# Kernel optimization log

Hardware: AMD Instinct MI355X
Metric: run time of the kernel (lower is better)

The kernel has to match this reference:

```python
import jax, jax.numpy as jnp
import numpy as np


def gcn_conv(x, edge_index, edge_weight, W, b):
    """PyG GCNConv: add self-loops (weight 1), symmetric normalization,
    linear transform, edge-weighted scatter-add aggregation, bias."""
    N = x.shape[0]
    src = jnp.concatenate([edge_index[0], jnp.arange(N, dtype=edge_index.dtype)])
    dst = jnp.concatenate([edge_index[1], jnp.arange(N, dtype=edge_index.dtype)])
    ew = jnp.concatenate([edge_weight, jnp.ones((N,), dtype=edge_weight.dtype)])
    # deg over destination nodes (source_to_target flow)
    deg = jax.ops.segment_sum(ew, dst, num_segments=N)
    dinv = jnp.where(deg > 0, deg ** -0.5, 0.0).astype(x.dtype)
    norm = dinv[src] * ew * dinv[dst]          # [E+N]
    xw = x @ W                                  # [N, out] linear first (cheaper)
    msgs = norm[:, None] * xw[src]              # [E+N, out]
    out = jax.ops.segment_sum(msgs, dst, num_segments=N)
    return out + b


def setup_inputs() -> dict:
    key = jax.random.key(0)
    ks = jax.random.split(key, 7)
    N, E, F_in, H, F_out = 100000, 1600000, 394, 256, 64
    x = jax.random.normal(ks[0], (N, F_in), dtype=jnp.float32)
    edge_index = jax.random.randint(ks[1], (2, E), 0, N, dtype=jnp.int32)
    edge_weight = jax.random.uniform(ks[2], (E,), dtype=jnp.float32)
    W1 = jax.random.normal(ks[3], (F_in, H), dtype=jnp.float32) * (1.0 / np.sqrt(F_in))
    b1 = jnp.zeros((H,), dtype=jnp.float32)
    W2 = jax.random.normal(ks[4], (H, F_out), dtype=jnp.float32) * (1.0 / np.sqrt(H))
    b2 = jnp.zeros((F_out,), dtype=jnp.float32)
    return {"x": x, "edge_index": edge_index, "edge_weight": edge_weight,
            "W1": W1, "b1": b1, "W2": W2, "b2": b2}


def reference(x, edge_index, edge_weight, W1, b1, W2, b2):
    h = gcn_conv(x, edge_index, edge_weight, W1, b1)
    h = jax.nn.relu(h)
    # F.dropout(training=self.training) is identity in eval mode
    out = gcn_conv(h, edge_index, edge_weight, W2, b2)
    return out
```

## Files before the change

kernel.cpp:

```cpp
#include <hip/hip_runtime.h>
#include <hip/hip_bf16.h>
#include <hip/hip_fp16.h>
#include <type_traits>


typedef _Float16 f16x8 __attribute__((ext_vector_type(8)));
typedef float f32x4 __attribute__((ext_vector_type(4)));

#define DEG_MASK ((1ull << 42) - 1)

__device__ inline void async_copy16(const void* g, void* l) {
    __builtin_amdgcn_global_load_lds(
        (const __attribute__((address_space(1))) void*)g,
        (__attribute__((address_space(3))) void*)l, 16, 0, 0);
}


__global__ __launch_bounds__(256) void setup(unsigned long long* packed, int N,
                                             const float* __restrict__ W1,
                                             __half* __restrict__ WT1,
                                             int K1, int N1, int Kpad1,
                                             const float* __restrict__ W2,
                                             __half* __restrict__ WT2,
                                             int K2, int N2, int Kpad2,
                                             int G0, int G1) {
    int b = blockIdx.x;
    if (b < G0) {
        int i = b * 256 + threadIdx.x;
        if (i < N) packed[i] = 0ull;
    } else if (b < G1) {
        int idx = (b - G0) * 256 + threadIdx.x;
        int total = N1 * Kpad1;
        if (idx < total) {
            int n = idx / Kpad1, k = idx % Kpad1;
            float v = (k < K1) ? W1[(size_t)k * N1 + n] : 0.0f;
            WT1[idx] = __float2half(v);
        }
    } else {
        int idx = (b - G1) * 256 + threadIdx.x;
        int total = N2 * Kpad2;
        if (idx < total) {
            int n = idx / Kpad2, k = idx % Kpad2;
            float v = (k < K2) ? W2[(size_t)k * N2 + n] : 0.0f;
            WT2[idx] = __float2half(v);
        }
    }
}

__global__ __launch_bounds__(256) void accum_deg_hist(const int* __restrict__ dst,
                                                      const float* __restrict__ ew,
                                                      unsigned long long* packed, int E) {
    int e = blockIdx.x * 256 + threadIdx.x;
    if (e < E) {
        int d = dst[e];
        unsigned long long add =
            (1ull << 42) + (unsigned long long)(ew[e] * 4294967296.0f);
        atomicAdd(&packed[d], add);
    }
}

#define SCAN_TILE 2048

__global__ __launch_bounds__(256) void scan1(const unsigned long long* __restrict__ packed,
                                             int* __restrict__ rowptr,
                                             float* __restrict__ dinv,
                                             int* __restrict__ bsums, int N) {
    __shared__ int tmp[256];
    int t = threadIdx.x;
    int base = blockIdx.x * SCAN_TILE + t * 8;
    int v[8], s = 0;
#pragma unroll
    for (int j = 0; j < 8; ++j) {
        int idx = base + j;
        if (idx < N) {
            unsigned long long pv = packed[idx];
            v[j] = (int)(pv >> 42);
            dinv[idx] = rsqrtf(1.0f + (float)(pv & DEG_MASK) * (1.0f / 4294967296.0f));
        } else v[j] = 0;
        s += v[j];
    }
    tmp[t] = s;
    __syncthreads();
#pragma unroll
    for (int off = 1; off < 256; off <<= 1) {
        int u = (t >= off) ? tmp[t - off] : 0;
        __syncthreads();
        tmp[t] += u;
        __syncthreads();
    }
    int run = tmp[t] - s;
#pragma unroll
    for (int j = 0; j < 8; ++j) {
        if (base + j < N) rowptr[base + j] = run;
        run += v[j];
    }
    if (t == 255) bsums[blockIdx.x] = tmp[255];
}

__global__ __launch_bounds__(256) void scan2(int* bsums, int* rowptr, int NB, int N, int E) {
    __shared__ int tmp[256];
    int t = threadIdx.x;
    int v = (t < NB) ? bsums[t] : 0;
    tmp[t] = v;
    __syncthreads();
#pragma unroll
    for (int off = 1; off < 256; off <<= 1) {
        int u = (t >= off) ? tmp[t - off] : 0;
        __syncthreads();
        tmp[t] += u;
        __syncthreads();
    }
    if (t < NB) bsums[t] = tmp[t] - v;
    if (t == 0) rowptr[N] = E;
}

__global__ __launch_bounds__(256) void scan3(int* rowptr, int* cursor,
                                             const int* __restrict__ bsums, int N) {
    int base = blockIdx.x * SCAN_TILE + threadIdx.x * 8;
    int off = bsums[blockIdx.x];
#pragma unroll
    for (int j = 0; j < 8; ++j)
        if (base + j < N) {
            int v = rowptr[base + j] + off;
            rowptr[base + j] = v;
            cursor[base + j] = v;
        }
}

template <int BM, int BN, int WARPS_M, int WARPS_N, int NT>
__global__ __launch_bounds__(NT) void gemm1_fill(const float* __restrict__ Ax,
                                                 const __half* __restrict__ BT,
                                                 __half* __restrict__ C,
                                                 int M, int K, int Kpad,
                                                 int GF,
                                                 const int* __restrict__ src,
                                                 const int* __restrict__ dst,
                                                 const float* __restrict__ ew,
                                                 const float* __restrict__ dinv,
                                                 int* __restrict__ cursor,
                                                 int2* __restrict__ cv, int E) {
    const int WM = BM / WARPS_M, WN = BN / WARPS_N;
    const int FM = WM / 16, FN = WN / 16;
    const int ACH = BM * 4;
    const int BCH = BN * 4;
    static_assert(ACH == NT, "1 A-chunk per thread");
    static_assert(BCH == 2 * NT, "2 B-chunks per thread");
    __shared__ __align__(16) __half lds[2][(ACH + BCH) * 8];

    if ((int)blockIdx.x < GF) {
        int e = blockIdx.x * NT + threadIdx.x;
        if (e < E) {
            int d = dst[e], s = src[e];
            int pos = atomicAdd(&cursor[d], 1);
            float v = dinv[s] * ew[e];
            cv[pos] = make_int2(s, __float_as_int(v));
        }
        return;
    }

    int tid = threadIdx.x;
    int lane = tid & 63;
    int w = tid >> 6;
    int wr = w / WARPS_N, wc = w % WARPS_N;
    int bm = (blockIdx.x - GF) * BM;
    int lrow = lane & 15;
    int lslot = lane >> 4;

    int arow = tid >> 2, ap = tid & 3;
    int aslot = ap ^ ((arow >> 1) & 3);
    int agrow = bm + arow; if (agrow >= M) agrow = M - 1;
    const float* abase = Ax + (size_t)agrow * K;

    const __half* bsrc[2];
#pragma unroll
    for (int i = 0; i < 2; ++i) {
        int c = tid + i * NT;
        int row = c >> 2, p = c & 3;
        bsrc[i] = BT + (size_t)row * Kpad + (size_t)((p ^ ((row >> 1) & 3)) * 8);
    }

    f32x4 acc[FM][FN];
#pragma unroll
    for (int m = 0; m < FM; ++m)
#pragma unroll
        for (int n = 0; n < FN; ++n) acc[m][n] = (f32x4){0.f, 0.f, 0.f, 0.f};

    float2 ar[4];
    auto loadA = [&](int s) {
        int gk = s * 32 + aslot * 8;
        if (gk + 8 <= K) {
            const float* p = abase + gk;
            ar[0] = *(const float2*)p;
            ar[1] = *(const float2*)(p + 2);
            ar[2] = *(const float2*)(p + 4);
            ar[3] = *(const float2*)(p + 6);
        } else {
            float t[8];
#pragma unroll
            for (int j = 0; j < 8; ++j) t[j] = (gk + j < K) ? abase[gk + j] : 0.0f;
            ar[0] = make_float2(t[0], t[1]);
            ar[1] = make_float2(t[2], t[3]);
            ar[2] = make_float2(t[4], t[5]);
            ar[3] = make_float2(t[6], t[7]);
        }
    };
    auto writeA = [&](int buf) {
        union { __half2 h[4]; uint4 u; } pk;
#pragma unroll
        for (int j = 0; j < 4; ++j) pk.h[j] = __floats2half2_rn(ar[j].x, ar[j].y);
        *(uint4*)&lds[buf][(size_t)tid * 8] = pk.u;
    };
    auto stageB = [&](int buf) {
#pragma unroll
        for (int i = 0; i < 2; ++i) {
            async_copy16(bsrc[i], &lds[buf][(size_t)((tid & ~63) + (i + 1) * NT) * 8]);
            bsrc[i] += 32;
        }
    };

    auto compute = [&](int buf) {
        f16x8 af[FM], bf[FN];
#pragma unroll
        for (int m = 0; m < FM; ++m) {
            int row = wr * WM + m * 16 + lrow;
            int p = lslot ^ ((row >> 1) & 3);
            af[m] = *(const f16x8*)&lds[buf][(size_t)(row * 4 + p) * 8];
        }
#pragma unroll
        for (int n = 0; n < FN; ++n) {
            int row = wc * WN + n * 16 + lrow;
            int p = lslot ^ ((row >> 1) & 3);
            bf[n] = *(const f16x8*)&lds[buf][(size_t)(ACH + row * 4 + p) * 8];
        }
#pragma unroll
        for (int m = 0; m < FM; ++m)
#pragma unroll
            for (int n = 0; n < FN; ++n)
                acc[m][n] = __builtin_amdgcn_mfma_f32_16x16x32_f16(af[m], bf[n], acc[m][n], 0, 0, 0);
    };

    const int nsteps = Kpad / 32;
    loadA(0);
    stageB(0);
    asm volatile("s_waitcnt vmcnt(2)" ::: "memory");
    writeA(0);
    asm volatile("s_waitcnt vmcnt(0) lgkmcnt(0)" ::: "memory");
    __builtin_amdgcn_s_barrier();
    for (int s = 0; s < nsteps; ++s) {
        bool more = (s + 1 < nsteps);
        if (more) { loadA(s + 1); stageB((s + 1) & 1); }
        compute(s & 1);
        if (more) {
            asm volatile("s_waitcnt vmcnt(2)" ::: "memory");
            writeA((s + 1) & 1);
            asm volatile("s_waitcnt vmcnt(0) lgkmcnt(0)" ::: "memory");
        }
        __builtin_amdgcn_s_barrier();
    }

    __syncthreads();
    {
        const int LW = WN + 8;
        __half* tile = (__half*)lds + (size_t)w * 16 * LW;
        const int CPR = WN / 8;
        const int CHT = (16 * CPR) / 64;
#pragma unroll
        for (int m = 0; m < FM; ++m) {
            int rb = bm + wr * WM + m * 16;
#pragma unroll
            for (int n = 0; n < FN; ++n)
#pragma unroll
                for (int i = 0; i < 4; ++i)
                    tile[((lane >> 4) * 4 + i) * LW + n * 16 + (lane & 15)] =
                        __float2half(acc[m][n][i]);
#pragma unroll
            for (int c = 0; c < CHT; ++c) {
                int ch = lane + c * 64;
                int r = ch / CPR, cc = ch % CPR;
                uint4 v = *(uint4*)&tile[r * LW + cc * 8];
                int grow = rb + r;
                if (grow < M)
                    *(uint4*)&C[(size_t)grow * BN + wc * WN + cc * 8] = v;
            }
        }
    }
}

template <int BM, int BN, int WARPS_M, int WARPS_N, int NT>
__global__ __launch_bounds__(NT) void gemm_f16(const __half* __restrict__ Ah,
                                               const __half* __restrict__ BT,
                                               __half* __restrict__ C,
                                               int M, int Kpad) {
    const int WM = BM / WARPS_M, WN = BN / WARPS_N;
    const int FM = WM / 16, FN = WN / 16;
    const int ACH = BM * 4;
    const int BCH = BN * 4;
    const int TOTCH = ACH + BCH;
    const int CH = TOTCH / NT;
    static_assert(CH == 3, "vmcnt(3) hardcoded below");
    __shared__ __align__(16) __half lds[2][TOTCH * 8];

    int tid = threadIdx.x;
    int lane = tid & 63;
    int w = tid >> 6;
    int wr = w / WARPS_N, wc = w % WARPS_N;
    int bm = blockIdx.x * BM;
    int lrow = lane & 15;
    int lslot = lane >> 4;

    const __half* srcp[CH];
#pragma unroll
    for (int i = 0; i < CH; ++i) {
        int ch = tid + i * NT;
        if (ch < ACH) {
            int c = ch, row = c >> 2;
            int grow = bm + row;
            if (grow >= M) grow = M - 1;
            srcp[i] = Ah + (size_t)grow * Kpad + (size_t)(((c & 3) ^ ((row >> 1) & 3)) * 8);
        } else {
            int c = ch - ACH, row = c >> 2;
            srcp[i] = BT + (size_t)row * Kpad + (size_t)(((c & 3) ^ ((row >> 1) & 3)) * 8);
        }
    }

    f32x4 acc[FM][FN];
#pragma unroll
    for (int m = 0; m < FM; ++m)
#pragma unroll
        for (int n = 0; n < FN; ++n) acc[m][n] = (f32x4){0.f, 0.f, 0.f, 0.f};

    auto stage = [&](int buf) {
#pragma unroll
        for (int i = 0; i < CH; ++i) {
            async_copy16(srcp[i], &lds[buf][(size_t)((tid & ~63) + i * NT) * 8]);
            srcp[i] += 32;
        }
    };

    auto compute = [&](int buf) {
        f16x8 af[FM], bf[FN];
#pragma unroll
        for (int m = 0; m < FM; ++m) {
            int row = wr * WM + m * 16 + lrow;
            int p = lslot ^ ((row >> 1) & 3);
            af[m] = *(const f16x8*)&lds[buf][(size_t)(row * 4 + p) * 8];
        }
#pragma unroll
        for (int n = 0; n < FN; ++n) {
            int row = wc * WN + n * 16 + lrow;
            int p = lslot ^ ((row >> 1) & 3);
            bf[n] = *(const f16x8*)&lds[buf][(size_t)(ACH + row * 4 + p) * 8];
        }
#pragma unroll
        for (int m = 0; m < FM; ++m)
#pragma unroll
            for (int n = 0; n < FN; ++n)
                acc[m][n] = __builtin_amdgcn_mfma_f32_16x16x32_f16(af[m], bf[n], acc[m][n], 0, 0, 0);
    };

    const int nsteps = Kpad / 32;
    stage(0);
    for (int s = 0; s < nsteps; ++s) {
        if (s + 1 < nsteps) {
            stage((s + 1) & 1);
            asm volatile("s_waitcnt vmcnt(3)" ::: "memory");
        } else {
            asm volatile("s_waitcnt vmcnt(0)" ::: "memory");
        }
        __builtin_amdgcn_s_barrier();
        compute(s & 1);
        __builtin_amdgcn_s_barrier();
    }

    __syncthreads();
    {
        const int LW = WN + 8;
        __half* tile = (__half*)lds + (size_t)w * 16 * LW;
        const int CPR = WN / 8;
        const int CHT = (16 * CPR) / 64;
#pragma unroll
        for (int m = 0; m < FM; ++m) {
            int rb = bm + wr * WM + m * 16;
#pragma unroll
            for (int n = 0; n < FN; ++n)
#pragma unroll
                for (int i = 0; i < 4; ++i)
                    tile[((lane >> 4) * 4 + i) * LW + n * 16 + (lane & 15)] =
                        __float2half(acc[m][n][i]);
#pragma unroll
            for (int c = 0; c < CHT; ++c) {
                int ch = lane + c * 64;
                int r = ch / CPR, cc = ch % CPR;
                uint4 v = *(uint4*)&tile[r * LW + cc * 8];
                int grow = rb + r;
                if (grow < M)
                    *(uint4*)&C[(size_t)grow * BN + wc * WN + cc * 8] = v;
            }
        }
    }
}

template <int F, int LPN, int RELU, typename OutT>
__global__ __launch_bounds__(256) void gatherh(const int* __restrict__ rowptr,
                                               const int2* __restrict__ cv,
                                               const __half* __restrict__ xw,
                                               const float* __restrict__ dinv,
                                               const float* __restrict__ bias,
                                               OutT* __restrict__ out, int N) {
    const int NPB = 256 / LPN;
    int d = blockIdx.x * NPB + threadIdx.x / LPN;
    if (d >= N) return;
    int lane = threadIdx.x % LPN;

    float di = dinv[d];
    uint2 raw = *(const uint2*)(xw + (size_t)d * F + lane * 4);
    float2 u0 = __half22float2(*(__half2*)&raw.x);
    float2 u1 = __half22float2(*(__half2*)&raw.y);
    float a0 = di * u0.x, a1 = di * u0.y, a2 = di * u1.x, a3 = di * u1.y;
    float b0 = 0.f, b1 = 0.f, b2 = 0.f, b3 = 0.f;

    int p = rowptr[d], p1 = rowptr[d + 1];
    for (; p + 4 <= p1; p += 4) {
        int2 e0 = cv[p], e1 = cv[p + 1], e2 = cv[p + 2], e3 = cv[p + 3];
        uint2 r0 = *(const uint2*)(xw + (size_t)e0.x * F + lane * 4);
        uint2 r1 = *(const uint2*)(xw + (size_t)e1.x * F + lane * 4);
        uint2 r2 = *(const uint2*)(xw + (size_t)e2.x * F + lane * 4);
        uint2 r3 = *(const uint2*)(xw + (size_t)e3.x * F + lane * 4);
        float w0 = __int_as_float(e0.y), w1 = __int_as_float(e1.y);
        float w2 = __int_as_float(e2.y), w3 = __int_as_float(e3.y);
        {
            float2 v0 = __half22float2(*(__half2*)&r0.x);
            float2 v1 = __half22float2(*(__half2*)&r0.y);
            a0 = fmaf(w0, v0.x, a0); a1 = fmaf(w0, v0.y, a1);
            a2 = fmaf(w0, v1.x, a2); a3 = fmaf(w0, v1.y, a3);
        }
        {
            float2 v0 = __half22float2(*(__half2*)&r1.x);
            float2 v1 = __half22float2(*(__half2*)&r1.y);
            b0 = fmaf(w1, v0.x, b0); b1 = fmaf(w1, v0.y, b1);
            b2 = fmaf(w1, v1.x, b2); b3 = fmaf(w1, v1.y, b3);
        }
        {
            float2 v0 = __half22float2(*(__half2*)&r2.x);
            float2 v1 = __half22float2(*(__half2*)&r2.y);
            a0 = fmaf(w2, v0.x, a0); a1 = fmaf(w2, v0.y, a1);
            a2 = fmaf(w2, v1.x, a2); a3 = fmaf(w2, v1.y, a3);
        }
        {
            float2 v0 = __half22float2(*(__half2*)&r3.x);
            float2 v1 = __half22float2(*(__half2*)&r3.y);
            b0 = fmaf(w3, v0.x, b0); b1 = fmaf(w3, v0.y, b1);
            b2 = fmaf(w3, v1.x, b2); b3 = fmaf(w3, v1.y, b3);
        }
    }
    for (; p < p1; ++p) {
        int2 e = cv[p];
        float wv = __int_as_float(e.y);
        uint2 rv = *(const uint2*)(xw + (size_t)e.x * F + lane * 4);
        float2 v0 = __half22float2(*(__half2*)&rv.x);
        float2 v1 = __half22float2(*(__half2*)&rv.y);
        a0 = fmaf(wv, v0.x, a0); a1 = fmaf(wv, v0.y, a1);
        a2 = fmaf(wv, v1.x, a2); a3 = fmaf(wv, v1.y, a3);
    }
    a0 += b0; a1 += b1; a2 += b2; a3 += b3;
    a0 *= di; a1 *= di; a2 *= di; a3 *= di;

    float4 bb = *(const float4*)&bias[lane * 4];
    a0 += bb.x; a1 += bb.y; a2 += bb.z; a3 += bb.w;
    if (RELU) {
        a0 = fmaxf(a0, 0.f); a1 = fmaxf(a1, 0.f);
        a2 = fmaxf(a2, 0.f); a3 = fmaxf(a3, 0.f);
    }
    if constexpr (std::is_same_v<OutT, float>) {
        *(float4*)&out[(size_t)d * F + lane * 4] = make_float4(a0, a1, a2, a3);
    } else {
        __half2 h0 = __floats2half2_rn(a0, a1);
        __half2 h1 = __floats2half2_rn(a2, a3);
        uint2 packed;
        packed.x = *(uint*)&h0;
        packed.y = *(uint*)&h1;
        *(uint2*)&out[(size_t)d * F + lane * 4] = packed;
    }
}

extern "C" void kernel_launch(void* const* d_in, const int* in_sizes, int n_in,
                              void* d_out, int out_size, void* d_ws, size_t ws_size,
                              hipStream_t stream) {
    const float* x  = (const float*)d_in[0];
    const int*   ei = (const int*)d_in[1];
    const float* ew = (const float*)d_in[2];
    const float* W1 = (const float*)d_in[3];
    const float* b1 = (const float*)d_in[4];
    const float* W2 = (const float*)d_in[5];
    const float* b2 = (const float*)d_in[6];
    float* out = (float*)d_out;

    const int H    = in_sizes[4];
    const int Fout = in_sizes[6];
    const int Fin  = in_sizes[3] / H;
    const int N    = in_sizes[0] / Fin;
    const int E    = in_sizes[2];

    const int Kpad1 = (Fin + 31) / 32 * 32;
    const int Kpad2 = (H + 31) / 32 * 32;

    const int* src = ei;
    const int* dst = ei + E;

    unsigned long long* packed = (unsigned long long*)d_ws;
    float* dinv   = (float*)(packed + N);
    int*   rowptr = (int*)(dinv + N);
    int*   cursor = rowptr + N + 4;
    int*   bsums  = cursor + N + 4;
    int2*  cv     = (int2*)(bsums + 256);
    __half* bufA  = (__half*)(cv + E);
    __half* bufB  = bufA + (size_t)N * H;
    __half* wt1   = bufB + (size_t)N * H;
    __half* wt2   = wt1 + (size_t)H * Kpad1;

    const int NB = (N + SCAN_TILE - 1) / SCAN_TILE;

    {
        int g0 = (N + 255) / 256;
        int g1 = (H * Kpad1 + 255) / 256;
        int g2 = (Fout * Kpad2 + 255) / 256;
        setup<<<g0 + g1 + g2, 256, 0, stream>>>(packed, N,
                                                W1, wt1, Fin, H, Kpad1,
                                                W2, wt2, H, Fout, Kpad2,
                                                g0, g0 + g1);
    }

    accum_deg_hist<<<(E + 255) / 256, 256, 0, stream>>>(dst, ew, packed, E);

    scan1<<<NB, 256, 0, stream>>>(packed, rowptr, dinv, bsums, N);
    scan2<<<1, 256, 0, stream>>>(bsums, rowptr, NB, N, E);
    scan3<<<NB, 256, 0, stream>>>(rowptr, cursor, bsums, N);

    {
        int GF = (E + 511) / 512;
        int G1 = (N + 127) / 128;
        gemm1_fill<128, 256, 2, 4, 512><<<GF + G1, 512, 0, stream>>>(
            x, wt1, bufA, N, Fin, Kpad1,
            GF, src, dst, ew, dinv, cursor, cv, E);
    }

    gatherh<256, 64, 1, __half><<<(N + 3) / 4, 256, 0, stream>>>(
        rowptr, cv, bufA, dinv, b1, bufB, N);

    gemm_f16<128, 64, 2, 2, 256><<<(N + 127) / 128, 256, 0, stream>>>(bufB, wt2, bufA, N, Kpad2);

    gatherh<64, 16, 0, float><<<(N + 15) / 16, 256, 0, stream>>>(
        rowptr, cv, bufA, dinv, b2, out, N);
}
```

Measured before the change: 450.4 us.

## Single-buffer A tile and restructure GEMM1 pipeline waits and barriers

```diff
diff --git a/kernel.cpp b/kernel.cpp
--- a/kernel.cpp
+++ b/kernel.cpp
@@ -145,7 +145,8 @@
     const int BCH = BN * 4;
     static_assert(ACH == NT, "1 A-chunk per thread");
     static_assert(BCH == 2 * NT, "2 B-chunks per thread");
-    __shared__ __align__(16) __half lds[2][(ACH + BCH) * 8];
+    __shared__ __align__(16) __half ldsA[ACH * 8];
+    __shared__ __align__(16) __half ldsB[2][BCH * 8];
 
     if ((int)blockIdx.x < GF) {
         int e = blockIdx.x * NT + threadIdx.x;
@@ -204,33 +205,33 @@
             ar[3] = make_float2(t[6], t[7]);
         }
     };
-    auto writeA = [&](int buf) {
+    auto writeA = [&]() {
         union { __half2 h[4]; uint4 u; } pk;
 #pragma unroll
         for (int j = 0; j < 4; ++j) pk.h[j] = __floats2half2_rn(ar[j].x, ar[j].y);
-        *(uint4*)&lds[buf][(size_t)tid * 8] = pk.u;
+        *(uint4*)&ldsA[(size_t)tid * 8] = pk.u;
     };
     auto stageB = [&](int buf) {
 #pragma unroll
         for (int i = 0; i < 2; ++i) {
-            async_copy16(bsrc[i], &lds[buf][(size_t)((tid & ~63) + (i + 1) * NT) * 8]);
+            async_copy16(bsrc[i], &ldsB[buf][(size_t)((tid & ~63) + i * NT) * 8]);
             bsrc[i] += 32;
         }
     };
 
-    auto compute = [&](int buf) {
+    auto compute = [&](int bbuf) {
         f16x8 af[FM], bf[FN];
 #pragma unroll
         for (int m = 0; m < FM; ++m) {
             int row = wr * WM + m * 16 + lrow;
             int p = lslot ^ ((row >> 1) & 3);
-            af[m] = *(const f16x8*)&lds[buf][(size_t)(row * 4 + p) * 8];
+            af[m] = *(const f16x8*)&ldsA[(size_t)(row * 4 + p) * 8];
         }
 #pragma unroll
         for (int n = 0; n < FN; ++n) {
             int row = wc * WN + n * 16 + lrow;
             int p = lslot ^ ((row >> 1) & 3);
-            bf[n] = *(const f16x8*)&lds[buf][(size_t)(ACH + row * 4 + p) * 8];
+            bf[n] = *(const f16x8*)&ldsB[bbuf][(size_t)(row * 4 + p) * 8];
         }
 #pragma unroll
         for (int m = 0; m < FM; ++m)
@@ -243,25 +244,37 @@
     loadA(0);
     stageB(0);
     asm volatile("s_waitcnt vmcnt(2)" ::: "memory");
-    writeA(0);
-    asm volatile("s_waitcnt vmcnt(0) lgkmcnt(0)" ::: "memory");
-    __builtin_amdgcn_s_barrier();
+    writeA();
+    asm volatile("s_waitcnt lgkmcnt(0)" ::: "memory");
+
     for (int s = 0; s < nsteps; ++s) {
         bool more = (s + 1 < nsteps);
-        if (more) { loadA(s + 1); stageB((s + 1) & 1); }
+        bool cnt = more && ((s + 1) * 32 + 32 <= K || (s + 1) * 32 >= K + 32);
+        if (more) {
+            loadA(s + 1);
+            stageB((s + 1) & 1);
+        }
+        if (more && cnt)
+            asm volatile("s_waitcnt vmcnt(6)" ::: "memory");
+        else
+            asm volatile("s_waitcnt vmcnt(0)" ::: "memory");
+        __builtin_amdgcn_s_barrier();
         compute(s & 1);
+        __builtin_amdgcn_s_barrier();
         if (more) {
-            asm volatile("s_waitcnt vmcnt(2)" ::: "memory");
-            writeA((s + 1) & 1);
-            asm volatile("s_waitcnt vmcnt(0) lgkmcnt(0)" ::: "memory");
-        }
-        __builtin_amdgcn_s_barrier();
+            if (cnt)
+                asm volatile("s_waitcnt vmcnt(2)" ::: "memory");
+            else
+                asm volatile("s_waitcnt vmcnt(0)" ::: "memory");
+            writeA();
+            asm volatile("s_waitcnt lgkmcnt(0)" ::: "memory");
+        }
     }
 
     __syncthreads();
     {
         const int LW = WN + 8;
-        __half* tile = (__half*)lds + (size_t)w * 16 * LW;
+        __half* tile = (__half*)ldsB + (size_t)w * 16 * LW;
         const int CPR = WN / 8;
         const int CHT = (16 * CPR) / 64;
 #pragma unroll
```

After: 457.4 us. No clear change (+1.6%).
